# Optimization experiments

Measured on AMD Instinct MI355X. Metric: run time of the kernel, lower is better.

## Reference

```python
import jax, jax.numpy as jnp
import numpy as np

N = 100000   # nodes
E = 1600000  # edges
D = 64       # in/hidden channels


def setup_inputs() -> dict:
    key = jax.random.key(0)
    ks = jax.random.split(key, 8)
    x = jax.random.normal(ks[0], (N, D), dtype=jnp.float32)
    edge_index = jax.random.randint(ks[1], (2, E), 0, N, dtype=jnp.int32)
    s = 1.0 / np.sqrt(D)
    W1 = jax.random.uniform(ks[2], (D, D), jnp.float32, -s, s)
    W2 = jax.random.uniform(ks[3], (D, D), jnp.float32, -s, s)
    W3 = jax.random.uniform(ks[4], (D, D), jnp.float32, -s, s)
    b1 = jnp.zeros((D,), jnp.float32)
    b2 = jnp.zeros((D,), jnp.float32)
    b3 = jnp.zeros((D,), jnp.float32)
    return {"x": x, "edge_index": edge_index,
            "W1": W1, "b1": b1, "W2": W2, "b2": b2, "W3": W3, "b3": b3}


def _gcn_conv(x, src, dst, deg_inv_sqrt, W, b):
    # norm = d^{-1/2}[src] * d^{-1/2}[dst] (symmetric GCN normalization w/ self-loops)
    norm = deg_inv_sqrt[src] * deg_inv_sqrt[dst]        # [E+N]
    h = x @ W                                           # [N, D] dense GEMM
    msg = h[src] * norm[:, None]                        # gather + scale
    out = jax.ops.segment_sum(msg, dst, num_segments=x.shape[0])  # scatter-add
    return out + b


def reference(x, edge_index, W1, b1, W2, b2, W3, b3):
    n = x.shape[0]
    loop = jnp.arange(n, dtype=edge_index.dtype)
    src = jnp.concatenate([edge_index[0], loop])        # add self-loops
    dst = jnp.concatenate([edge_index[1], loop])
    deg = jax.ops.segment_sum(jnp.ones_like(src, x.dtype), dst, num_segments=n)
    deg_inv_sqrt = jnp.where(deg > 0, jax.lax.rsqrt(jnp.maximum(deg, 1.0)), 0.0)

    h = _gcn_conv(x, src, dst, deg_inv_sqrt, W1, b1)
    h = jax.nn.relu(h)                                  # dropout is identity (eval)
    h = _gcn_conv(h, src, dst, deg_inv_sqrt, W2, b2)
    h = jax.nn.relu(h)
    out = _gcn_conv(h, src, dst, deg_inv_sqrt, W3, b3)
    return out
```

## Files before the change

kernel.cpp:

```cpp
#include <hip/hip_runtime.h>
#include <hip/hip_fp16.h>
#include <type_traits>

#define DCH 64
#define NBSHIFT 8
#define BROWS 256
#define MAXNB 512
#define CAPB 5120
#define CAP 8192
#define CHUNK 4096

__global__ void init_cursor(int* __restrict__ cursor, int NB) {
    int i = blockIdx.x * blockDim.x + threadIdx.x;
    if (i < NB) cursor[i] = i * CAPB;
}

__global__ __launch_bounds__(256) void bucket_scatter(const int* __restrict__ src,
        const int* __restrict__ dst, int* __restrict__ cursor,
        unsigned int* __restrict__ tmp, int E, int NB) {
    __shared__ int hist[MAXNB];
    __shared__ int res[MAXNB];
    const int base_e = blockIdx.x * CHUNK;
    const int nloc = min(CHUNK, E - base_e);
    for (int i = threadIdx.x; i < NB; i += blockDim.x) hist[i] = 0;
    __syncthreads();
    for (int i = threadIdx.x; i < nloc; i += blockDim.x)
        atomicAdd(&hist[dst[base_e + i] >> NBSHIFT], 1);
    __syncthreads();
    for (int i = threadIdx.x; i < NB; i += blockDim.x) {
        int c = hist[i];
        res[i] = c ? atomicAdd(&cursor[i], c) : 0;
        hist[i] = 0;
    }
    __syncthreads();
    for (int i = threadIdx.x; i < nloc; i += blockDim.x) {
        int d = dst[base_e + i];
        int b = d >> NBSHIFT;
        int r = atomicAdd(&hist[b], 1);
        unsigned int packed = ((unsigned int)(d & (BROWS - 1)) << 24) |
                              (unsigned int)src[base_e + i];
        tmp[res[b] + r] = packed;
    }
}

__global__ __launch_bounds__(BROWS) void bucket_to_csr(
        const unsigned int* __restrict__ tmp, const int* __restrict__ cursor,
        int* __restrict__ rowbeg, int* __restrict__ rowend,
        int* __restrict__ srcs, float* __restrict__ dinv, int N) {
    __shared__ int hist[BROWS];
    __shared__ int off[BROWS];
    __shared__ int cur[BROWS];
    __shared__ int stage[CAP];
    const int b = blockIdx.x;
    const int base = b * CAPB;
    const int count = cursor[b] - base;
    const int t = threadIdx.x;
    hist[t] = 0;
    __syncthreads();
    for (int i = t; i < count; i += BROWS)
        atomicAdd(&hist[tmp[base + i] >> 24], 1);
    __syncthreads();
    int v = hist[t];
    off[t] = v;
    __syncthreads();
    for (int o = 1; o < BROWS; o <<= 1) {
        int add = (t >= o) ? off[t - o] : 0;
        __syncthreads();
        off[t] += add;
        __syncthreads();
    }
    int excl = off[t] - v;
    cur[t] = excl;
    int node = (b << NBSHIFT) + t;
    if (node < N) {
        rowbeg[node] = base + excl;
        rowend[node] = base + excl + v;
        dinv[node]   = rsqrtf((float)v + 1.0f);
    }
    __syncthreads();
    const bool st = (count <= CAP);
    for (int i = t; i < count; i += BROWS) {
        unsigned int p = tmp[base + i];
        int low = p >> 24;
        int s = (int)(p & 0xFFFFFFu);
        int pos = atomicAdd(&cur[low], 1);
        if (st) stage[pos] = s;
        else    srcs[base + pos] = s;
    }
    __syncthreads();
    if (st)
        for (int i = t; i < count; i += BROWS) srcs[base + i] = stage[i];
}

template<typename InT>
__global__ __launch_bounds__(256, 4) void gemm64(const InT* __restrict__ A,
        const float* __restrict__ W, const float* __restrict__ dinv,
        __half* __restrict__ H, int nrows) {
    __shared__ float Wl[64 * 64];
    __shared__ float Al[64 * 68];
    #pragma unroll
    for (int j = 0; j < 4; ++j) {
        int idx = (int)threadIdx.x + j * 256;
        float4 w = ((const float4*)W)[idx];
        int k = idx >> 4, c = (idx & 15) * 4;
        *(float4*)&Wl[k * 64 + c] = w;
    }
    const int tx = threadIdx.x & 15;
    const int ty = threadIdx.x >> 4;
    const int c0 = tx * 4, r0 = ty * 4;
    const int ntiles = (nrows + 63) >> 6;
    for (int tile = blockIdx.x; tile < ntiles; tile += gridDim.x) {
        const int rowbase = tile << 6;
        const int rmax = min(64, nrows - rowbase);
        __syncthreads();
        #pragma unroll
        for (int j = 0; j < 4; ++j) {
            int idx = (int)threadIdx.x + j * 256;
            int r = idx >> 4, kq = idx & 15;
            float4 a;
            if (r < rmax) {
                if constexpr (std::is_same<InT, float>::value) {
                    a = *(const float4*)(A + (size_t)(rowbase + r) * 64 + kq * 4);
                } else {
                    unsigned long long u = *(const unsigned long long*)
                        ((const __half*)A + (size_t)(rowbase + r) * 64 + kq * 4);
                    union { unsigned long long u; __half2 h[2]; } cv; cv.u = u;
                    float2 f0 = __half22float2(cv.h[0]);
                    float2 f1 = __half22float2(cv.h[1]);
                    a = make_float4(f0.x, f0.y, f1.x, f1.y);
                }
            } else a = make_float4(0.f, 0.f, 0.f, 0.f);
            *(float4*)&Al[r * 68 + kq * 4] = a;
        }
        __syncthreads();
        float acc[4][4] = {};
        #pragma unroll 8
        for (int k = 0; k < 64; ++k) {
            float4 wv = *(const float4*)&Wl[k * 64 + c0];
            float a0 = Al[(r0 + 0) * 68 + k];
            float a1 = Al[(r0 + 1) * 68 + k];
            float a2 = Al[(r0 + 2) * 68 + k];
            float a3 = Al[(r0 + 3) * 68 + k];
            acc[0][0] += a0 * wv.x; acc[0][1] += a0 * wv.y; acc[0][2] += a0 * wv.z; acc[0][3] += a0 * wv.w;
            acc[1][0] += a1 * wv.x; acc[1][1] += a1 * wv.y; acc[1][2] += a1 * wv.z; acc[1][3] += a1 * wv.w;
            acc[2][0] += a2 * wv.x; acc[2][1] += a2 * wv.y; acc[2][2] += a2 * wv.z; acc[2][3] += a2 * wv.w;
            acc[3][0] += a3 * wv.x; acc[3][1] += a3 * wv.y; acc[3][2] += a3 * wv.z; acc[3][3] += a3 * wv.w;
        }
        #pragma unroll
        for (int i = 0; i < 4; ++i) {
            int r = r0 + i;
            if (r < rmax) {
                float s = dinv[rowbase + r];
                __half2* ph = (__half2*)(H + (size_t)(rowbase + r) * 64 + c0);
                ph[0] = __floats2half2_rn(acc[i][0] * s, acc[i][1] * s);
                ph[1] = __floats2half2_rn(acc[i][2] * s, acc[i][3] * s);
            }
        }
    }
}

__device__ __forceinline__ void accumh(__half2 acc[4], float4 v) {
    const __half2* hp = (const __half2*)&v;
    #pragma unroll
    for (int j = 0; j < 4; ++j) acc[j] = __hadd2(acc[j], hp[j]);
}

__device__ __forceinline__ float4 row16(const __half* __restrict__ hs, int s, int q) {
    return *(const float4*)((const char*)hs + ((size_t)s << 7) + (q << 4));
}

template<typename OutT>
__global__ __launch_bounds__(256) void aggregate(
    const __half* __restrict__ hs, const int* __restrict__ rowbeg,
    const int* __restrict__ rowend, const int* __restrict__ srcs,
    const float* __restrict__ dinv, const float* __restrict__ b,
    OutT* __restrict__ out, int n, int do_relu)
{
    int wid  = (blockIdx.x * blockDim.x + threadIdx.x) >> 6;
    int lane = threadIdx.x & 63;
    if (wid >= n) return;
    const int g = lane >> 3;
    const int q = lane & 7;
    int beg = rowbeg[wid], end = rowend[wid];
    __half2 zero = __float2half2_rn(0.f);
    __half2 acch[4]  = {zero, zero, zero, zero};
    __half2 acch2[4] = {zero, zero, zero, zero};
    if (g == 7) accumh(acch, row16(hs, wid, q));
    int e = beg + g;
    for (; e + 8 < end; e += 16) {
        int s0 = srcs[e];
        int s1 = srcs[e + 8];
        float4 v0 = row16(hs, s0, q);
        float4 v1 = row16(hs, s1, q);
        accumh(acch, v0);
        accumh(acch2, v1);
    }
    if (e < end) accumh(acch, row16(hs, srcs[e], q));
    float acc[8];
    #pragma unroll
    for (int j = 0; j < 4; ++j) {
        float2 f0 = __half22float2(acch[j]);
        float2 f1 = __half22float2(acch2[j]);
        acc[2 * j]     = f0.x + f1.x;
        acc[2 * j + 1] = f0.y + f1.y;
    }
    #pragma unroll
    for (int j = 0; j < 8; ++j) {
        float a = acc[j];
        a += __shfl_xor(a, 8);
        a += __shfl_xor(a, 16);
        a += __shfl_xor(a, 32);
        acc[j] = a;
    }
    if (g == 0) {
        float dd = dinv[wid];
        float o[8];
        #pragma unroll
        for (int j = 0; j < 8; ++j) {
            float v = acc[j] * dd + b[q * 8 + j];
            o[j] = do_relu ? fmaxf(v, 0.f) : v;
        }
        if constexpr (std::is_same<OutT, __half>::value) {
            union { uint4 u; __half2 h[4]; } cv;
            cv.h[0] = __floats2half2_rn(o[0], o[1]);
            cv.h[1] = __floats2half2_rn(o[2], o[3]);
            cv.h[2] = __floats2half2_rn(o[4], o[5]);
            cv.h[3] = __floats2half2_rn(o[6], o[7]);
            *(uint4*)((__half*)out + (size_t)wid * DCH + q * 8) = cv.u;
        } else {
            float4* po = (float4*)((float*)out + (size_t)wid * DCH + q * 8);
            po[0] = make_float4(o[0], o[1], o[2], o[3]);
            po[1] = make_float4(o[4], o[5], o[6], o[7]);
        }
    }
}

extern "C" void kernel_launch(void* const* d_in, const int* in_sizes, int n_in,
                              void* d_out, int out_size, void* d_ws, size_t ws_size,
                              hipStream_t stream) {
    const float* x  = (const float*)d_in[0];
    const int*   ei = (const int*)d_in[1];
    const float* W1 = (const float*)d_in[2];
    const float* b1 = (const float*)d_in[3];
    const float* W2 = (const float*)d_in[4];
    const float* b2 = (const float*)d_in[5];
    const float* W3 = (const float*)d_in[6];
    const float* b3 = (const float*)d_in[7];

    const int N = in_sizes[0] / DCH;
    const int E = in_sizes[1] / 2;
    const int* src = ei;
    const int* dst = ei + E;
    const int NB = (N + BROWS - 1) >> NBSHIFT;

    char* ws = (char*)d_ws;
    size_t off = 0;
    auto alloc = [&](size_t bytes) { void* p = ws + off; off = (off + bytes + 255) & ~(size_t)255; return p; };
    int*    cursor = (int*)   alloc((size_t)MAXNB * 4);
    int*    rowbeg = (int*)   alloc((size_t)N * 4);
    int*    rowend = (int*)   alloc((size_t)N * 4);
    int*    srcs   = (int*)   alloc((size_t)NB * CAPB * 4);
    float*  dinv   = (float*) alloc((size_t)N * 4);
    __half* hs     = (__half*)alloc((size_t)N * DCH * 2);
    __half* agg    = (__half*)alloc((size_t)N * DCH * 2);
    unsigned int* tmp = (unsigned int*)hs;
    float* out = (float*)d_out;

    const int T = 256;
    const int gAG  = (N * DCH + T - 1) / T;
    const int gGM  = (N + 63) / 64;
    const int nchk = (E + CHUNK - 1) / CHUNK;

    init_cursor<<<(NB + T - 1) / T, T, 0, stream>>>(cursor, NB);
    bucket_scatter<<<nchk, T, 0, stream>>>(src, dst, cursor, tmp, E, NB);
    bucket_to_csr<<<NB, BROWS, 0, stream>>>(tmp, cursor, rowbeg, rowend, srcs, dinv, N);

    gemm64<float><<<gGM, T, 0, stream>>>(x, W1, dinv, hs, N);
    aggregate<__half><<<gAG, T, 0, stream>>>(hs, rowbeg, rowend, srcs, dinv, b1, agg, N, 1);

    gemm64<__half><<<gGM, T, 0, stream>>>(agg, W2, dinv, hs, N);
    aggregate<__half><<<gAG, T, 0, stream>>>(hs, rowbeg, rowend, srcs, dinv, b2, agg, N, 1);

    gemm64<__half><<<gGM, T, 0, stream>>>(agg, W3, dinv, hs, N);
    aggregate<float><<<gAG, T, 0, stream>>>(hs, rowbeg, rowend, srcs, dinv, b3, out, N, 0);
}
```

Measured before the change: 229.0 us.

## Fuse next-layer GEMM into aggregation epilogue and unroll gather four-way

Layers 2 and 3 no longer run a separate GEMM. The aggregation kernel now applies bias and ReLU, then multiplies each node row by the next weight matrix. The weights are held transposed as half precision in shared memory, and the row is broadcast across the wavefront with shuffles. This removes two GEMM launches and the round trip of an intermediate half tensor through memory. The gather loop now keeps four independent accumulators and clamps indices with masking to increase memory-level parallelism, and the bucket scatter chunk size is halved. In exchange there is extra shuffle work per node, weights stored in fp16, and 512-thread blocks that each reload the weights.

```diff
diff --git a/kernel.cpp b/kernel.cpp
--- a/kernel.cpp
+++ b/kernel.cpp
@@ -1,6 +1,5 @@
 #include <hip/hip_runtime.h>
 #include <hip/hip_fp16.h>
-#include <type_traits>
 
 #define DCH 64
 #define NBSHIFT 8
@@ -8,7 +7,7 @@
 #define MAXNB 512
 #define CAPB 5120
 #define CAP 8192
-#define CHUNK 4096
+#define CHUNK 2048
 
 __global__ void init_cursor(int* __restrict__ cursor, int NB) {
     int i = blockIdx.x * blockDim.x + threadIdx.x;
@@ -92,8 +91,7 @@
         for (int i = t; i < count; i += BROWS) srcs[base + i] = stage[i];
 }
 
-template<typename InT>
-__global__ __launch_bounds__(256, 4) void gemm64(const InT* __restrict__ A,
+__global__ __launch_bounds__(256, 4) void gemm64(const float* __restrict__ A,
         const float* __restrict__ W, const float* __restrict__ dinv,
         __half* __restrict__ H, int nrows) {
     __shared__ float Wl[64 * 64];
@@ -117,19 +115,8 @@
         for (int j = 0; j < 4; ++j) {
             int idx = (int)threadIdx.x + j * 256;
             int r = idx >> 4, kq = idx & 15;
-            float4 a;
-            if (r < rmax) {
-                if constexpr (std::is_same<InT, float>::value) {
-                    a = *(const float4*)(A + (size_t)(rowbase + r) * 64 + kq * 4);
-                } else {
-                    unsigned long long u = *(const unsigned long long*)
-                        ((const __half*)A + (size_t)(rowbase + r) * 64 + kq * 4);
-                    union { unsigned long long u; __half2 h[2]; } cv; cv.u = u;
-                    float2 f0 = __half22float2(cv.h[0]);
-                    float2 f1 = __half22float2(cv.h[1]);
-                    a = make_float4(f0.x, f0.y, f1.x, f1.y);
-                }
-            } else a = make_float4(0.f, 0.f, 0.f, 0.f);
+            float4 a = (r < rmax) ? *(const float4*)(A + (size_t)(rowbase + r) * 64 + kq * 4)
+                                  : make_float4(0.f, 0.f, 0.f, 0.f);
             *(float4*)&Al[r * 68 + kq * 4] = a;
         }
         __syncthreads();
@@ -169,40 +156,38 @@
     return *(const float4*)((const char*)hs + ((size_t)s << 7) + (q << 4));
 }
 
-template<typename OutT>
-__global__ __launch_bounds__(256) void aggregate(
-    const __half* __restrict__ hs, const int* __restrict__ rowbeg,
-    const int* __restrict__ rowend, const int* __restrict__ srcs,
-    const float* __restrict__ dinv, const float* __restrict__ b,
-    OutT* __restrict__ out, int n, int do_relu)
+__device__ __forceinline__ float4 maskf4(float4 v, bool p) {
+    return make_float4(p ? v.x : 0.f, p ? v.y : 0.f, p ? v.z : 0.f, p ? v.w : 0.f);
+}
+
+__device__ __forceinline__ void gather_reduce(
+    const __half* __restrict__ hs, const int* __restrict__ srcs,
+    int beg, int end, int g, int q, int wid, float acc[8])
 {
-    int wid  = (blockIdx.x * blockDim.x + threadIdx.x) >> 6;
-    int lane = threadIdx.x & 63;
-    if (wid >= n) return;
-    const int g = lane >> 3;
-    const int q = lane & 7;
-    int beg = rowbeg[wid], end = rowend[wid];
-    __half2 zero = __float2half2_rn(0.f);
-    __half2 acch[4]  = {zero, zero, zero, zero};
-    __half2 acch2[4] = {zero, zero, zero, zero};
-    if (g == 7) accumh(acch, row16(hs, wid, q));
-    int e = beg + g;
-    for (; e + 8 < end; e += 16) {
-        int s0 = srcs[e];
-        int s1 = srcs[e + 8];
+    __half2 z = __float2half2_rn(0.f);
+    __half2 A[4] = {z,z,z,z}, B[4] = {z,z,z,z}, C[4] = {z,z,z,z}, D[4] = {z,z,z,z};
+    if (g == 7) accumh(A, row16(hs, wid, q));
+    for (int e = beg + g; e < end; e += 32) {
+        int last = end - 1;
+        int i1 = min(e + 8,  last);
+        int i2 = min(e + 16, last);
+        int i3 = min(e + 24, last);
+        int s0 = srcs[e], s1 = srcs[i1], s2 = srcs[i2], s3 = srcs[i3];
         float4 v0 = row16(hs, s0, q);
         float4 v1 = row16(hs, s1, q);
-        accumh(acch, v0);
-        accumh(acch2, v1);
-    }
-    if (e < end) accumh(acch, row16(hs, srcs[e], q));
-    float acc[8];
+        float4 v2 = row16(hs, s2, q);
+        float4 v3 = row16(hs, s3, q);
+        accumh(A, v0);
+        accumh(B, maskf4(v1, e + 8  < end));
+        accumh(C, maskf4(v2, e + 16 < end));
+        accumh(D, maskf4(v3, e + 24 < end));
+    }
     #pragma unroll
     for (int j = 0; j < 4; ++j) {
-        float2 f0 = __half22float2(acch[j]);
-        float2 f1 = __half22float2(acch2[j]);
-        acc[2 * j]     = f0.x + f1.x;
-        acc[2 * j + 1] = f0.y + f1.y;
+        __half2 s = __hadd2(__hadd2(A[j], B[j]), __hadd2(C[j], D[j]));
+        float2 f = __half22float2(s);
+        acc[2 * j]     = f.x;
+        acc[2 * j + 1] = f.y;
     }
     #pragma unroll
     for (int j = 0; j < 8; ++j) {
@@ -212,26 +197,66 @@
         a += __shfl_xor(a, 32);
         acc[j] = a;
     }
+}
+
+__global__ __launch_bounds__(512, 8) void agg_fused(
+    const __half* __restrict__ hs, const int* __restrict__ rowbeg,
+    const int* __restrict__ rowend, const int* __restrict__ srcs,
+    const float* __restrict__ dinv, const float* __restrict__ bia,
+    const float* __restrict__ Wn, __half* __restrict__ hnext, int n)
+{
+    __shared__ __half Wt[64][68];
+    for (int i = threadIdx.x; i < 4096; i += 512) {
+        int k = i >> 6, c = i & 63;
+        Wt[c][k] = __float2half(Wn[i]);
+    }
+    __syncthreads();
+    int wid = (int)((blockIdx.x * 512 + threadIdx.x) >> 6);
+    if (wid >= n) return;
+    int lane = threadIdx.x & 63;
+    int g = lane >> 3, q = lane & 7;
+    float acc[8];
+    gather_reduce(hs, srcs, rowbeg[wid], rowend[wid], g, q, wid, acc);
+    float dd = dinv[wid];
+    float v[8];
+    #pragma unroll
+    for (int j = 0; j < 8; ++j)
+        v[j] = fmaxf(acc[j] * dd + bia[q * 8 + j], 0.f);
+    float o = 0.f;
+    #pragma unroll
+    for (int ko = 0; ko < 8; ++ko) {
+        #pragma unroll
+        for (int j = 0; j < 8; j += 2) {
+            float r0 = __shfl(v[j],     ko);
+            float r1 = __shfl(v[j + 1], ko);
+            __half2 w2 = *(const __half2*)&Wt[lane][ko * 8 + j];
+            float2 wf = __half22float2(w2);
+            o += r0 * wf.x + r1 * wf.y;
+        }
+    }
+    hnext[(size_t)wid * DCH + lane] = __float2half(o * dd);
+}
+
+__global__ __launch_bounds__(256) void agg_final(
+    const __half* __restrict__ hs, const int* __restrict__ rowbeg,
+    const int* __restrict__ rowend, const int* __restrict__ srcs,
+    const float* __restrict__ dinv, const float* __restrict__ b,
+    float* __restrict__ out, int n)
+{
+    int wid  = (blockIdx.x * blockDim.x + threadIdx.x) >> 6;
+    if (wid >= n) return;
+    int lane = threadIdx.x & 63;
+    int g = lane >> 3, q = lane & 7;
+    float acc[8];
+    gather_reduce(hs, srcs, rowbeg[wid], rowend[wid], g, q, wid, acc);
     if (g == 0) {
         float dd = dinv[wid];
         float o[8];
         #pragma unroll
-        for (int j = 0; j < 8; ++j) {
-            float v = acc[j] * dd + b[q * 8 + j];
-            o[j] = do_relu ? fmaxf(v, 0.f) : v;
-        }
-        if constexpr (std::is_same<OutT, __half>::value) {
-            union { uint4 u; __half2 h[4]; } cv;
-            cv.h[0] = __floats2half2_rn(o[0], o[1]);
-            cv.h[1] = __floats2half2_rn(o[2], o[3]);
-            cv.h[2] = __floats2half2_rn(o[4], o[5]);
-            cv.h[3] = __floats2half2_rn(o[6], o[7]);
-            *(uint4*)((__half*)out + (size_t)wid * DCH + q * 8) = cv.u;
-        } else {
-            float4* po = (float4*)((float*)out + (size_t)wid * DCH + q * 8);
-            po[0] = make_float4(o[0], o[1], o[2], o[3]);
-            po[1] = make_float4(o[4], o[5], o[6], o[7]);
-        }
+        for (int j = 0; j < 8; ++j) o[j] = acc[j] * dd + b[q * 8 + j];
+        float4* po = (float4*)(out + (size_t)wid * DCH + q * 8);
+        po[0] = make_float4(o[0], o[1], o[2], o[3]);
+        po[1] = make_float4(o[4], o[5], o[6], o[7]);
     }
 }
 
@@ -261,13 +286,14 @@
     int*    rowend = (int*)   alloc((size_t)N * 4);
     int*    srcs   = (int*)   alloc((size_t)NB * CAPB * 4);
     float*  dinv   = (float*) alloc((size_t)N * 4);
-    __half* hs     = (__half*)alloc((size_t)N * DCH * 2);
-    __half* agg    = (__half*)alloc((size_t)N * DCH * 2);
-    unsigned int* tmp = (unsigned int*)hs;
+    __half* hs1    = (__half*)alloc((size_t)N * DCH * 2);
+    __half* hs2    = (__half*)alloc((size_t)N * DCH * 2);
+    unsigned int* tmp = (unsigned int*)hs1;
     float* out = (float*)d_out;
 
     const int T = 256;
-    const int gAG  = (N * DCH + T - 1) / T;
+    const int gAGf = (N + 7) / 8;
+    const int gAGl = (N * DCH + T - 1) / T;
     const int gGM  = (N + 63) / 64;
     const int nchk = (E + CHUNK - 1) / CHUNK;
 
@@ -275,12 +301,11 @@
     bucket_scatter<<<nchk, T, 0, stream>>>(src, dst, cursor, tmp, E, NB);
     bucket_to_csr<<<NB, BROWS, 0, stream>>>(tmp, cursor, rowbeg, rowend, srcs, dinv, N);
 
-    gemm64<float><<<gGM, T, 0, stream>>>(x, W1, dinv, hs, N);
-    aggregate<__half><<<gAG, T, 0, stream>>>(hs, rowbeg, rowend, srcs, dinv, b1, agg, N, 1);
-
-    gemm64<__half><<<gGM, T, 0, stream>>>(agg, W2, dinv, hs, N);
-    aggregate<__half><<<gAG, T, 0, stream>>>(hs, rowbeg, rowend, srcs, dinv, b2, agg, N, 1);
-
-    gemm64<__half><<<gGM, T, 0, stream>>>(agg, W3, dinv, hs, N);
-    aggregate<float><<<gAG, T, 0, stream>>>(hs, rowbeg, rowend, srcs, dinv, b3, out, N, 0);
-}
+    gemm64<<<gGM, T, 0, stream>>>(x, W1, dinv, hs1, N);
+
+    agg_fused<<<gAGf, 512, 0, stream>>>(hs1, rowbeg, rowend, srcs, dinv, b1, W2, hs2, N);
+
+    agg_fused<<<gAGf, 512, 0, stream>>>(hs2, rowbeg, rowend, srcs, dinv, b2, W3, hs1, N);
+
+    agg_final<<<gAGl, T, 0, stream>>>(hs1, rowbeg, rowend, srcs, dinv, b3, out, N);
+}
```

Result: slower. 339.4 us (+48.2%).

## Fuse aggregation with next layer's GEMM and drop cursor init kernel

Applied to the files above, without the earlier changes.

Each intermediate layer now runs a single kernel that gathers and aggregates neighbor rows for a 128-row tile, applies bias and ReLU, and keeps the result in shared memory. It then multiplies that tile by the next weight matrix and writes the pre-scaled half-precision features. This removes the intermediate activation round trip through global memory and two kernel launches per layer, and the aggregate stays in fp32 instead of being rounded to half. The cursor init kernel is replaced by a memset, with the bucket base offset added at use. In exchange, each 512-thread block runs 16 sequential gather rounds before a barrier, and heavy shared memory use (about 51 KB) may limit occupancy for the latency-bound gather.

```diff
diff --git a/kernel.cpp b/kernel.cpp
--- a/kernel.cpp
+++ b/kernel.cpp
@@ -1,6 +1,5 @@
 #include <hip/hip_runtime.h>
 #include <hip/hip_fp16.h>
-#include <type_traits>
 
 #define DCH 64
 #define NBSHIFT 8
@@ -9,11 +8,6 @@
 #define CAPB 5120
 #define CAP 8192
 #define CHUNK 4096
-
-__global__ void init_cursor(int* __restrict__ cursor, int NB) {
-    int i = blockIdx.x * blockDim.x + threadIdx.x;
-    if (i < NB) cursor[i] = i * CAPB;
-}
 
 __global__ __launch_bounds__(256) void bucket_scatter(const int* __restrict__ src,
         const int* __restrict__ dst, int* __restrict__ cursor,
@@ -29,7 +23,7 @@
     __syncthreads();
     for (int i = threadIdx.x; i < NB; i += blockDim.x) {
         int c = hist[i];
-        res[i] = c ? atomicAdd(&cursor[i], c) : 0;
+        res[i] = c ? (i * CAPB + atomicAdd(&cursor[i], c)) : 0;
         hist[i] = 0;
     }
     __syncthreads();
@@ -53,7 +47,7 @@
     __shared__ int stage[CAP];
     const int b = blockIdx.x;
     const int base = b * CAPB;
-    const int count = cursor[b] - base;
+    const int count = cursor[b];
     const int t = threadIdx.x;
     hist[t] = 0;
     __syncthreads();
@@ -92,8 +86,7 @@
         for (int i = t; i < count; i += BROWS) srcs[base + i] = stage[i];
 }
 
-template<typename InT>
-__global__ __launch_bounds__(256, 4) void gemm64(const InT* __restrict__ A,
+__global__ __launch_bounds__(256, 4) void gemm64(const float* __restrict__ A,
         const float* __restrict__ W, const float* __restrict__ dinv,
         __half* __restrict__ H, int nrows) {
     __shared__ float Wl[64 * 64];
@@ -102,8 +95,7 @@
     for (int j = 0; j < 4; ++j) {
         int idx = (int)threadIdx.x + j * 256;
         float4 w = ((const float4*)W)[idx];
-        int k = idx >> 4, c = (idx & 15) * 4;
-        *(float4*)&Wl[k * 64 + c] = w;
+        *(float4*)&Wl[(idx >> 4) * 64 + (idx & 15) * 4] = w;
     }
     const int tx = threadIdx.x & 15;
     const int ty = threadIdx.x >> 4;
@@ -117,19 +109,8 @@
         for (int j = 0; j < 4; ++j) {
             int idx = (int)threadIdx.x + j * 256;
             int r = idx >> 4, kq = idx & 15;
-            float4 a;
-            if (r < rmax) {
-                if constexpr (std::is_same<InT, float>::value) {
-                    a = *(const float4*)(A + (size_t)(rowbase + r) * 64 + kq * 4);
-                } else {
-                    unsigned long long u = *(const unsigned long long*)
-                        ((const __half*)A + (size_t)(rowbase + r) * 64 + kq * 4);
-                    union { unsigned long long u; __half2 h[2]; } cv; cv.u = u;
-                    float2 f0 = __half22float2(cv.h[0]);
-                    float2 f1 = __half22float2(cv.h[1]);
-                    a = make_float4(f0.x, f0.y, f1.x, f1.y);
-                }
-            } else a = make_float4(0.f, 0.f, 0.f, 0.f);
+            float4 a = (r < rmax) ? *(const float4*)(A + (size_t)(rowbase + r) * 64 + kq * 4)
+                                  : make_float4(0.f, 0.f, 0.f, 0.f);
             *(float4*)&Al[r * 68 + kq * 4] = a;
         }
         __syncthreads();
@@ -169,18 +150,122 @@
     return *(const float4*)((const char*)hs + ((size_t)s << 7) + (q << 4));
 }
 
-template<typename OutT>
-__global__ __launch_bounds__(256) void aggregate(
+__global__ __launch_bounds__(512, 6) void fused_layer(
+    const __half* __restrict__ hs, const int* __restrict__ rowbeg,
+    const int* __restrict__ rowend, const int* __restrict__ srcs,
+    const float* __restrict__ dinv, const float* __restrict__ bia,
+    const float* __restrict__ W, __half* __restrict__ hnext, int n)
+{
+    __shared__ float Wl[64 * 64];
+    __shared__ float Al[128 * 68];
+    #pragma unroll
+    for (int j = 0; j < 2; ++j) {
+        int idx = (int)threadIdx.x + j * 512;
+        float4 w = ((const float4*)W)[idx];
+        *(float4*)&Wl[(idx >> 4) * 64 + (idx & 15) * 4] = w;
+    }
+    const int rowbase = blockIdx.x << 7;
+    const int wv   = threadIdx.x >> 6;
+    const int lane = threadIdx.x & 63;
+    const int g = lane >> 3, q = lane & 7;
+    float bv[8];
+    #pragma unroll
+    for (int j = 0; j < 8; ++j) bv[j] = bia[q * 8 + j];
+
+    for (int rep = 0; rep < 16; ++rep) {
+        const int r = rep * 8 + wv;
+        const int wid = rowbase + r;
+        const bool valid = wid < n;
+        float acc[8];
+        if (valid) {
+            int beg = rowbeg[wid], end = rowend[wid];
+            __half2 zero = __float2half2_rn(0.f);
+            __half2 acch[4]  = {zero, zero, zero, zero};
+            __half2 acch2[4] = {zero, zero, zero, zero};
+            if (g == 7) accumh(acch, row16(hs, wid, q));
+            int e = beg + g;
+            for (; e + 8 < end; e += 16) {
+                int s0 = srcs[e];
+                int s1 = srcs[e + 8];
+                float4 v0 = row16(hs, s0, q);
+                float4 v1 = row16(hs, s1, q);
+                accumh(acch, v0);
+                accumh(acch2, v1);
+            }
+            if (e < end) accumh(acch, row16(hs, srcs[e], q));
+            #pragma unroll
+            for (int j = 0; j < 4; ++j) {
+                float2 f0 = __half22float2(acch[j]);
+                float2 f1 = __half22float2(acch2[j]);
+                acc[2 * j]     = f0.x + f1.x;
+                acc[2 * j + 1] = f0.y + f1.y;
+            }
+            #pragma unroll
+            for (int j = 0; j < 8; ++j) {
+                float a = acc[j];
+                a += __shfl_xor(a, 8);
+                a += __shfl_xor(a, 16);
+                a += __shfl_xor(a, 32);
+                acc[j] = a;
+            }
+        }
+        if (g == 0) {
+            float4 o0 = make_float4(0.f, 0.f, 0.f, 0.f), o1 = o0;
+            if (valid) {
+                float dd = dinv[wid];
+                o0.x = fmaxf(acc[0] * dd + bv[0], 0.f);
+                o0.y = fmaxf(acc[1] * dd + bv[1], 0.f);
+                o0.z = fmaxf(acc[2] * dd + bv[2], 0.f);
+                o0.w = fmaxf(acc[3] * dd + bv[3], 0.f);
+                o1.x = fmaxf(acc[4] * dd + bv[4], 0.f);
+                o1.y = fmaxf(acc[5] * dd + bv[5], 0.f);
+                o1.z = fmaxf(acc[6] * dd + bv[6], 0.f);
+                o1.w = fmaxf(acc[7] * dd + bv[7], 0.f);
+            }
+            *(float4*)&Al[r * 68 + q * 8]     = o0;
+            *(float4*)&Al[r * 68 + q * 8 + 4] = o1;
+        }
+    }
+    __syncthreads();
+    const int tx = threadIdx.x & 15;
+    const int ty = threadIdx.x >> 4;
+    const int c0 = tx * 4, r0 = ty * 4;
+    float acc2[4][4] = {};
+    #pragma unroll 8
+    for (int k = 0; k < 64; ++k) {
+        float4 wv4 = *(const float4*)&Wl[k * 64 + c0];
+        float a0 = Al[(r0 + 0) * 68 + k];
+        float a1 = Al[(r0 + 1) * 68 + k];
+        float a2 = Al[(r0 + 2) * 68 + k];
+        float a3 = Al[(r0 + 3) * 68 + k];
+        acc2[0][0] += a0 * wv4.x; acc2[0][1] += a0 * wv4.y; acc2[0][2] += a0 * wv4.z; acc2[0][3] += a0 * wv4.w;
+        acc2[1][0] += a1 * wv4.x; acc2[1][1] += a1 * wv4.y; acc2[1][2] += a1 * wv4.z; acc2[1][3] += a1 * wv4.w;
+        acc2[2][0] += a2 * wv4.x; acc2[2][1] += a2 * wv4.y; acc2[2][2] += a2 * wv4.z; acc2[2][3] += a2 * wv4.w;
+        acc2[3][0] += a3 * wv4.x; acc2[3][1] += a3 * wv4.y; acc2[3][2] += a3 * wv4.z; acc2[3][3] += a3 * wv4.w;
+    }
+    const int rmax = min(128, n - rowbase);
+    #pragma unroll
+    for (int i = 0; i < 4; ++i) {
+        int r = r0 + i;
+        if (r < rmax) {
+            float s = dinv[rowbase + r];
+            __half2* ph = (__half2*)(hnext + (size_t)(rowbase + r) * 64 + c0);
+            ph[0] = __floats2half2_rn(acc2[i][0] * s, acc2[i][1] * s);
+            ph[1] = __floats2half2_rn(acc2[i][2] * s, acc2[i][3] * s);
+        }
+    }
+}
+
+__global__ __launch_bounds__(256) void agg_final(
     const __half* __restrict__ hs, const int* __restrict__ rowbeg,
     const int* __restrict__ rowend, const int* __restrict__ srcs,
     const float* __restrict__ dinv, const float* __restrict__ b,
-    OutT* __restrict__ out, int n, int do_relu)
+    float* __restrict__ out, int n)
 {
     int wid  = (blockIdx.x * blockDim.x + threadIdx.x) >> 6;
+    if (wid >= n) return;
     int lane = threadIdx.x & 63;
-    if (wid >= n) return;
-    const int g = lane >> 3;
-    const int q = lane & 7;
+    const int g = lane >> 3, q = lane & 7;
     int beg = rowbeg[wid], end = rowend[wid];
     __half2 zero = __float2half2_rn(0.f);
     __half2 acch[4]  = {zero, zero, zero, zero};
@@ -216,22 +301,10 @@
         float dd = dinv[wid];
         float o[8];
         #pragma unroll
-        for (int j = 0; j < 8; ++j) {
-            float v = acc[j] * dd + b[q * 8 + j];
-            o[j] = do_relu ? fmaxf(v, 0.f) : v;
-        }
-        if constexpr (std::is_same<OutT, __half>::value) {
-            union { uint4 u; __half2 h[4]; } cv;
-            cv.h[0] = __floats2half2_rn(o[0], o[1]);
-            cv.h[1] = __floats2half2_rn(o[2], o[3]);
-            cv.h[2] = __floats2half2_rn(o[4], o[5]);
-            cv.h[3] = __floats2half2_rn(o[6], o[7]);
-            *(uint4*)((__half*)out + (size_t)wid * DCH + q * 8) = cv.u;
-        } else {
-            float4* po = (float4*)((float*)out + (size_t)wid * DCH + q * 8);
-            po[0] = make_float4(o[0], o[1], o[2], o[3]);
-            po[1] = make_float4(o[4], o[5], o[6], o[7]);
-        }
+        for (int j = 0; j < 8; ++j) o[j] = acc[j] * dd + b[q * 8 + j];
+        float4* po = (float4*)(out + (size_t)wid * DCH + q * 8);
+        po[0] = make_float4(o[0], o[1], o[2], o[3]);
+        po[1] = make_float4(o[4], o[5], o[6], o[7]);
     }
 }
 
@@ -261,26 +334,26 @@
     int*    rowend = (int*)   alloc((size_t)N * 4);
     int*    srcs   = (int*)   alloc((size_t)NB * CAPB * 4);
     float*  dinv   = (float*) alloc((size_t)N * 4);
-    __half* hs     = (__half*)alloc((size_t)N * DCH * 2);
-    __half* agg    = (__half*)alloc((size_t)N * DCH * 2);
-    unsigned int* tmp = (unsigned int*)hs;
+    __half* hs1    = (__half*)alloc((size_t)N * DCH * 2);
+    __half* hs2    = (__half*)alloc((size_t)N * DCH * 2);
+    unsigned int* tmp = (unsigned int*)hs1;
     float* out = (float*)d_out;
 
     const int T = 256;
-    const int gAG  = (N * DCH + T - 1) / T;
+    const int gAGl = (N * DCH + T - 1) / T;
+    const int gFU  = (N + 127) / 128;
     const int gGM  = (N + 63) / 64;
     const int nchk = (E + CHUNK - 1) / CHUNK;
 
-    init_cursor<<<(NB + T - 1) / T, T, 0, stream>>>(cursor, NB);
+    hipMemsetAsync(cursor, 0, (size_t)NB * 4, stream);
     bucket_scatter<<<nchk, T, 0, stream>>>(src, dst, cursor, tmp, E, NB);
     bucket_to_csr<<<NB, BROWS, 0, stream>>>(tmp, cursor, rowbeg, rowend, srcs, dinv, N);
 
-    gemm64<float><<<gGM, T, 0, stream>>>(x, W1, dinv, hs, N);
-    aggregate<__half><<<gAG, T, 0, stream>>>(hs, rowbeg, rowend, srcs, dinv, b1, agg, N, 1);
-
-    gemm64<__half><<<gGM, T, 0, stream>>>(agg, W2, dinv, hs, N);
-    aggregate<__half><<<gAG, T, 0, stream>>>(hs, rowbeg, rowend, srcs, dinv, b2, agg, N, 1);
-
-    gemm64<__half><<<gGM, T, 0, stream>>>(agg, W3, dinv, hs, N);
-    aggregate<float><<<gAG, T, 0, stream>>>(hs, rowbeg, rowend, srcs, dinv, b3, out, N, 0);
-}
+    gemm64<<<gGM, T, 0, stream>>>(x, W1, dinv, hs1, N);
+
+    fused_layer<<<gFU, 512, 0, stream>>>(hs1, rowbeg, rowend, srcs, dinv, b1, W2, hs2, N);
+
+    fused_layer<<<gFU, 512, 0, stream>>>(hs2, rowbeg, rowend, srcs, dinv, b2, W3, hs1, N);
+
+    agg_final<<<gAGl, T, 0, stream>>>(hs1, rowbeg, rowend, srcs, dinv, b3, out, N);
+}
```

Measured after the change: 281.5 us. 22.9% more time.
